# Kernel tuning notes

Hardware: AMD Instinct MI355X
Metric: run time of the kernel (lower is better)

## Reference

```python
import jax, jax.numpy as jnp
import numpy as np

N, S, C, K, V = 8, 2048, 4, 512, 64


def setup_inputs() -> dict:
    key = jax.random.key(0)
    kx, ke = jax.random.split(key)
    x = jax.random.normal(kx, (N, S, C, V), dtype=jnp.float32)
    # nn.Parameter(torch.rand(...)) -> uniform [0,1)
    embedding = jax.random.uniform(ke, (C, K, V), dtype=jnp.float32)
    return {"x": x, "embedding": embedding}


def reference(x, embedding):
    n, s, c, v = x.shape
    xf = x.reshape(n * s, c, v)  # (NS, C, V)
    x2 = jnp.sum(xf * xf, axis=-1, keepdims=True)           # (NS, C, 1)
    e2 = jnp.sum(embedding * embedding, axis=-1)            # (C, K)
    xe = jnp.einsum('ncv,ckv->nck', xf, embedding)          # (NS, C, K)
    d2 = x2 - 2.0 * xe + e2[None]                           # (NS, C, K)
    index = jnp.argmin(d2, axis=2)                          # (NS, C)
    # gather: output[n, c] = embedding[c, index[n, c]]
    output = embedding[jnp.arange(c)[None, :], index]       # (NS, C, V)
    output = output.reshape(x.shape)
    out0 = jax.lax.stop_gradient(output - x) + x            # straight-through
    d1 = jax.lax.stop_gradient(x) - output
    out1 = jnp.sum(d1 * d1, axis=3)                         # (N, S, C)
    d2_ = x - jax.lax.stop_gradient(output)
    out2 = jnp.sum(d2_ * d2_, axis=3)                       # (N, S, C)
    return (out0, out1, out2)
```

## Files before the change

kernel.cpp:

```cpp
#include <hip/hip_runtime.h>

#define NROW 16384
#define CCH  4
#define KCB  512
#define VDIM 64
#define KO   4096

typedef __attribute__((ext_vector_type(8))) short  short8;
typedef __attribute__((ext_vector_type(4))) float  floatx4;

__device__ inline unsigned short bf16h(float v, float* rem) {
    unsigned u = __float_as_uint(v);
    unsigned r = u + 0x7FFFu + ((u >> 16) & 1u);
    unsigned short h = (unsigned short)(r >> 16);
    *rem = v - __uint_as_float((unsigned)h << 16);
    return h;
}

__global__ __launch_bounds__(512, 1)
void vq_fused(const float* __restrict__ x, const float* __restrict__ emb,
              float* __restrict__ out) {
    extern __shared__ unsigned short smem[];
    unsigned short* bhi = smem;
    unsigned short* blo = smem + 32768;
    float* e2s = (float*)(smem + 65536);

    const int tid  = threadIdx.x;
    const int lane = tid & 63;
    const int m    = lane & 15;
    const int quad = lane >> 4;
    const int wave = tid >> 6;
    const int c    = blockIdx.y;
    const int rbase = blockIdx.x * 256 + wave * 32;

    const float* embc = emb + (size_t)c * (KCB * VDIM);

    {
        const int cb = wave * 64;
#pragma unroll
        for (int j = 0; j < 16; ++j) {
            const int g = cb * 16 + j * 64 + lane;
            const float4 t = ((const float4*)embc)[g];
            const int code = cb + j * 4 + quad;
            const int koct = m >> 1, half = m & 1;
            ushort4 h4, l4; float r, d;
            h4.x = bf16h(t.x, &r); l4.x = bf16h(r, &d);
            h4.y = bf16h(t.y, &r); l4.y = bf16h(r, &d);
            h4.z = bf16h(t.z, &r); l4.z = bf16h(r, &d);
            h4.w = bf16h(t.w, &r); l4.w = bf16h(r, &d);
            const int off = (koct * 512 + code) * 8 + half * 4;
            *(ushort4*)&bhi[off] = h4;
            *(ushort4*)&blo[off] = l4;
            float s = 0.f;
            s = fmaf(t.x, t.x, s); s = fmaf(t.y, t.y, s);
            s = fmaf(t.z, t.z, s); s = fmaf(t.w, t.w, s);
            s += __shfl_xor(s, 1, 64);
            s += __shfl_xor(s, 2, 64);
            s += __shfl_xor(s, 4, 64);
            s += __shfl_xor(s, 8, 64);
            if (m == 0) e2s[code] = s;
        }
    }

    short8 ah[2][2], al[2][2];
#pragma unroll
    for (int g = 0; g < 2; ++g) {
        const int row = rbase + g * 16 + m;
        const float4* xr = (const float4*)(x + ((size_t)row * CCH + c) * VDIM);
#pragma unroll
        for (int h = 0; h < 2; ++h) {
            const float4 f0 = xr[h * 8 + quad * 2];
            const float4 f1 = xr[h * 8 + quad * 2 + 1];
            const float fv[8] = {f0.x, f0.y, f0.z, f0.w, f1.x, f1.y, f1.z, f1.w};
            short8 hh, ll;
#pragma unroll
            for (int j = 0; j < 8; ++j) {
                float r, d;
                hh[j] = (short)bf16h(fv[j], &r);
                ll[j] = (short)bf16h(r, &d);
            }
            ah[g][h] = hh; al[g][h] = ll;
        }
    }

    __syncthreads();

    float bd[2][4]; int bkk[2][4];
#pragma unroll
    for (int g = 0; g < 2; ++g)
#pragma unroll
        for (int j = 0; j < 4; ++j) { bd[g][j] = 3.4e38f; bkk[g][j] = 0; }

#pragma unroll 4
    for (int t = 0; t < KCB / 16; ++t) {
        const int code = t * 16 + m;
        const unsigned short* ph = bhi + (size_t)(quad * 512 + code) * 8;
        const unsigned short* pl = blo + (size_t)(quad * 512 + code) * 8;
        const short8 bh0 = *(const short8*)ph;
        const short8 bh1 = *(const short8*)(ph + 4 * KO);
        const short8 bl0 = *(const short8*)pl;
        const short8 bl1 = *(const short8*)(pl + 4 * KO);
        const float e2v = e2s[code];

        floatx4 acch0 = {0.f,0.f,0.f,0.f}, acch1 = {0.f,0.f,0.f,0.f};
        floatx4 accm0 = {0.f,0.f,0.f,0.f}, accm1 = {0.f,0.f,0.f,0.f};
        acch0 = __builtin_amdgcn_mfma_f32_16x16x32_bf16(ah[0][0], bh0, acch0, 0, 0, 0);
        acch1 = __builtin_amdgcn_mfma_f32_16x16x32_bf16(ah[1][0], bh0, acch1, 0, 0, 0);
        accm0 = __builtin_amdgcn_mfma_f32_16x16x32_bf16(ah[0][0], bl0, accm0, 0, 0, 0);
        accm1 = __builtin_amdgcn_mfma_f32_16x16x32_bf16(ah[1][0], bl0, accm1, 0, 0, 0);
        acch0 = __builtin_amdgcn_mfma_f32_16x16x32_bf16(ah[0][1], bh1, acch0, 0, 0, 0);
        acch1 = __builtin_amdgcn_mfma_f32_16x16x32_bf16(ah[1][1], bh1, acch1, 0, 0, 0);
        accm0 = __builtin_amdgcn_mfma_f32_16x16x32_bf16(al[0][0], bh0, accm0, 0, 0, 0);
        accm1 = __builtin_amdgcn_mfma_f32_16x16x32_bf16(al[1][0], bh0, accm1, 0, 0, 0);
        accm0 = __builtin_amdgcn_mfma_f32_16x16x32_bf16(ah[0][1], bl1, accm0, 0, 0, 0);
        accm1 = __builtin_amdgcn_mfma_f32_16x16x32_bf16(ah[1][1], bl1, accm1, 0, 0, 0);
        accm0 = __builtin_amdgcn_mfma_f32_16x16x32_bf16(al[0][1], bh1, accm0, 0, 0, 0);
        accm1 = __builtin_amdgcn_mfma_f32_16x16x32_bf16(al[1][1], bh1, accm1, 0, 0, 0);

#pragma unroll
        for (int j = 0; j < 4; ++j) {
            const float d0 = fmaf(-2.0f, acch0[j] + accm0[j], e2v);
            const float d1 = fmaf(-2.0f, acch1[j] + accm1[j], e2v);
            if (d0 < bd[0][j]) { bd[0][j] = d0; bkk[0][j] = code; }
            if (d1 < bd[1][j]) { bd[1][j] = d1; bkk[1][j] = code; }
        }
    }

#pragma unroll
    for (int g = 0; g < 2; ++g)
#pragma unroll
    for (int j = 0; j < 4; ++j) {
        float d = bd[g][j]; int k = bkk[g][j];
#pragma unroll
        for (int mask = 1; mask < 16; mask <<= 1) {
            const float od = __shfl_xor(d, mask, 64);
            const int   ok = __shfl_xor(k, mask, 64);
            if (od < d || (od == d && ok < k)) { d = od; k = ok; }
        }
        bd[g][j] = d; bkk[g][j] = k;
    }

    const size_t base1 = (size_t)NROW * CCH * VDIM;
    const size_t base2 = base1 + (size_t)NROW * CCH;
#pragma unroll
    for (int g = 0; g < 2; ++g)
#pragma unroll
    for (int j = 0; j < 4; ++j) {
        const int row  = rbase + g * 16 + quad * 4 + j;
        const int code = bkk[g][j];
        const float4 t4 = ((const float4*)(x + ((size_t)row * CCH + c) * VDIM))[m];
        const float4 e4 = ((const float4*)(embc + (size_t)code * VDIM))[m];
        float4 w;
        w.x = (e4.x - t4.x) + t4.x;
        w.y = (e4.y - t4.y) + t4.y;
        w.z = (e4.z - t4.z) + t4.z;
        w.w = (e4.w - t4.w) + t4.w;
        ((float4*)(out + ((size_t)row * CCH + c) * VDIM))[m] = w;
        float s = 0.f, dx;
        dx = t4.x - e4.x; s = fmaf(dx, dx, s);
        dx = t4.y - e4.y; s = fmaf(dx, dx, s);
        dx = t4.z - e4.z; s = fmaf(dx, dx, s);
        dx = t4.w - e4.w; s = fmaf(dx, dx, s);
        s += __shfl_xor(s, 1, 64);
        s += __shfl_xor(s, 2, 64);
        s += __shfl_xor(s, 4, 64);
        s += __shfl_xor(s, 8, 64);
        if (m == 0) {
            const size_t idx = (size_t)row * CCH + c;
            out[base1 + idx] = s;
            out[base2 + idx] = s;
        }
    }
}

extern "C" void kernel_launch(void* const* d_in, const int* in_sizes, int n_in,
                              void* d_out, int out_size, void* d_ws, size_t ws_size,
                              hipStream_t stream) {
    const float* x   = (const float*)d_in[0];
    const float* emb = (const float*)d_in[1];
    float* out = (float*)d_out;
    const size_t lds_bytes = 65536u * 2u + 512u * 4u;
    vq_fused<<<dim3(NROW / 256, CCH), dim3(512), lds_bytes, stream>>>(x, emb, out);
}
```

Baseline: 92.62 us.

## Drop codebook low-part bf16 split, halve rows per block, XOR-swizzle LDS

```diff
diff --git a/kernel.cpp b/kernel.cpp
--- a/kernel.cpp
+++ b/kernel.cpp
@@ -4,7 +4,6 @@
 #define CCH  4
 #define KCB  512
 #define VDIM 64
-#define KO   4096
 
 typedef __attribute__((ext_vector_type(8))) short  short8;
 typedef __attribute__((ext_vector_type(4))) float  floatx4;
@@ -16,14 +15,17 @@
     *rem = v - __uint_as_float((unsigned)h << 16);
     return h;
 }
+__device__ inline unsigned short bf16r(float v) {
+    unsigned u = __float_as_uint(v);
+    return (unsigned short)((u + 0x7FFFu + ((u >> 16) & 1u)) >> 16);
+}
 
-__global__ __launch_bounds__(512, 1)
+__global__ __launch_bounds__(512, 4)
 void vq_fused(const float* __restrict__ x, const float* __restrict__ emb,
               float* __restrict__ out) {
     extern __shared__ unsigned short smem[];
-    unsigned short* bhi = smem;
-    unsigned short* blo = smem + 32768;
-    float* e2s = (float*)(smem + 65536);
+    unsigned short* eh = smem;
+    float* e2s = (float*)(smem + 32768);
 
     const int tid  = threadIdx.x;
     const int lane = tid & 63;
@@ -31,26 +33,23 @@
     const int quad = lane >> 4;
     const int wave = tid >> 6;
     const int c    = blockIdx.y;
-    const int rbase = blockIdx.x * 256 + wave * 32;
+    const int rbase = blockIdx.x * 128 + wave * 16;
 
     const float* embc = emb + (size_t)c * (KCB * VDIM);
 
     {
         const int cb = wave * 64;
+        const int koct = m >> 1, half = m & 1;
 #pragma unroll
         for (int j = 0; j < 16; ++j) {
             const int g = cb * 16 + j * 64 + lane;
             const float4 t = ((const float4*)embc)[g];
             const int code = cb + j * 4 + quad;
-            const int koct = m >> 1, half = m & 1;
-            ushort4 h4, l4; float r, d;
-            h4.x = bf16h(t.x, &r); l4.x = bf16h(r, &d);
-            h4.y = bf16h(t.y, &r); l4.y = bf16h(r, &d);
-            h4.z = bf16h(t.z, &r); l4.z = bf16h(r, &d);
-            h4.w = bf16h(t.w, &r); l4.w = bf16h(r, &d);
-            const int off = (koct * 512 + code) * 8 + half * 4;
-            *(ushort4*)&bhi[off] = h4;
-            *(ushort4*)&blo[off] = l4;
+            ushort4 h4;
+            h4.x = bf16r(t.x); h4.y = bf16r(t.y);
+            h4.z = bf16r(t.z); h4.w = bf16r(t.w);
+            const int off = (koct * 512 + (code ^ koct)) * 8 + half * 4;
+            *(ushort4*)&eh[off] = h4;
             float s = 0.f;
             s = fmaf(t.x, t.x, s); s = fmaf(t.y, t.y, s);
             s = fmaf(t.z, t.z, s); s = fmaf(t.w, t.w, s);
@@ -62,10 +61,9 @@
         }
     }
 
-    short8 ah[2][2], al[2][2];
-#pragma unroll
-    for (int g = 0; g < 2; ++g) {
-        const int row = rbase + g * 16 + m;
+    short8 ah[2], al[2];
+    {
+        const int row = rbase + m;
         const float4* xr = (const float4*)(x + ((size_t)row * CCH + c) * VDIM);
 #pragma unroll
         for (int h = 0; h < 2; ++h) {
@@ -79,75 +77,57 @@
                 hh[j] = (short)bf16h(fv[j], &r);
                 ll[j] = (short)bf16h(r, &d);
             }
-            ah[g][h] = hh; al[g][h] = ll;
+            ah[h] = hh; al[h] = ll;
         }
     }
 
     __syncthreads();
 
-    float bd[2][4]; int bkk[2][4];
+    float bd[4]; int bkk[4];
 #pragma unroll
-    for (int g = 0; g < 2; ++g)
-#pragma unroll
-        for (int j = 0; j < 4; ++j) { bd[g][j] = 3.4e38f; bkk[g][j] = 0; }
+    for (int j = 0; j < 4; ++j) { bd[j] = 3.4e38f; bkk[j] = 0; }
+
+    const int mq0 = m ^ quad;
+    const int mq1 = m ^ (quad + 4);
 
 #pragma unroll 4
     for (int t = 0; t < KCB / 16; ++t) {
         const int code = t * 16 + m;
-        const unsigned short* ph = bhi + (size_t)(quad * 512 + code) * 8;
-        const unsigned short* pl = blo + (size_t)(quad * 512 + code) * 8;
-        const short8 bh0 = *(const short8*)ph;
-        const short8 bh1 = *(const short8*)(ph + 4 * KO);
-        const short8 bl0 = *(const short8*)pl;
-        const short8 bl1 = *(const short8*)(pl + 4 * KO);
+        const short8 bh0 = *(const short8*)&eh[( quad      * 512 + t * 16 + mq0) * 8];
+        const short8 bh1 = *(const short8*)&eh[((quad + 4) * 512 + t * 16 + mq1) * 8];
         const float e2v = e2s[code];
 
-        floatx4 acch0 = {0.f,0.f,0.f,0.f}, acch1 = {0.f,0.f,0.f,0.f};
-        floatx4 accm0 = {0.f,0.f,0.f,0.f}, accm1 = {0.f,0.f,0.f,0.f};
-        acch0 = __builtin_amdgcn_mfma_f32_16x16x32_bf16(ah[0][0], bh0, acch0, 0, 0, 0);
-        acch1 = __builtin_amdgcn_mfma_f32_16x16x32_bf16(ah[1][0], bh0, acch1, 0, 0, 0);
-        accm0 = __builtin_amdgcn_mfma_f32_16x16x32_bf16(ah[0][0], bl0, accm0, 0, 0, 0);
-        accm1 = __builtin_amdgcn_mfma_f32_16x16x32_bf16(ah[1][0], bl0, accm1, 0, 0, 0);
-        acch0 = __builtin_amdgcn_mfma_f32_16x16x32_bf16(ah[0][1], bh1, acch0, 0, 0, 0);
-        acch1 = __builtin_amdgcn_mfma_f32_16x16x32_bf16(ah[1][1], bh1, acch1, 0, 0, 0);
-        accm0 = __builtin_amdgcn_mfma_f32_16x16x32_bf16(al[0][0], bh0, accm0, 0, 0, 0);
-        accm1 = __builtin_amdgcn_mfma_f32_16x16x32_bf16(al[1][0], bh0, accm1, 0, 0, 0);
-        accm0 = __builtin_amdgcn_mfma_f32_16x16x32_bf16(ah[0][1], bl1, accm0, 0, 0, 0);
-        accm1 = __builtin_amdgcn_mfma_f32_16x16x32_bf16(ah[1][1], bl1, accm1, 0, 0, 0);
-        accm0 = __builtin_amdgcn_mfma_f32_16x16x32_bf16(al[0][1], bh1, accm0, 0, 0, 0);
-        accm1 = __builtin_amdgcn_mfma_f32_16x16x32_bf16(al[1][1], bh1, accm1, 0, 0, 0);
+        floatx4 acc0 = {0.f,0.f,0.f,0.f}, acc1 = {0.f,0.f,0.f,0.f};
+        acc0 = __builtin_amdgcn_mfma_f32_16x16x32_bf16(ah[0], bh0, acc0, 0, 0, 0);
+        acc1 = __builtin_amdgcn_mfma_f32_16x16x32_bf16(al[0], bh0, acc1, 0, 0, 0);
+        acc0 = __builtin_amdgcn_mfma_f32_16x16x32_bf16(ah[1], bh1, acc0, 0, 0, 0);
+        acc1 = __builtin_amdgcn_mfma_f32_16x16x32_bf16(al[1], bh1, acc1, 0, 0, 0);
 
 #pragma unroll
         for (int j = 0; j < 4; ++j) {
-            const float d0 = fmaf(-2.0f, acch0[j] + accm0[j], e2v);
-            const float d1 = fmaf(-2.0f, acch1[j] + accm1[j], e2v);
-            if (d0 < bd[0][j]) { bd[0][j] = d0; bkk[0][j] = code; }
-            if (d1 < bd[1][j]) { bd[1][j] = d1; bkk[1][j] = code; }
+            const float d0 = fmaf(-2.0f, acc0[j] + acc1[j], e2v);
+            if (d0 < bd[j]) { bd[j] = d0; bkk[j] = code; }
         }
     }
 
 #pragma unroll
-    for (int g = 0; g < 2; ++g)
-#pragma unroll
     for (int j = 0; j < 4; ++j) {
-        float d = bd[g][j]; int k = bkk[g][j];
+        float d = bd[j]; int k = bkk[j];
 #pragma unroll
         for (int mask = 1; mask < 16; mask <<= 1) {
             const float od = __shfl_xor(d, mask, 64);
             const int   ok = __shfl_xor(k, mask, 64);
             if (od < d || (od == d && ok < k)) { d = od; k = ok; }
         }
-        bd[g][j] = d; bkk[g][j] = k;
+        bd[j] = d; bkk[j] = k;
     }
 
     const size_t base1 = (size_t)NROW * CCH * VDIM;
     const size_t base2 = base1 + (size_t)NROW * CCH;
 #pragma unroll
-    for (int g = 0; g < 2; ++g)
-#pragma unroll
     for (int j = 0; j < 4; ++j) {
-        const int row  = rbase + g * 16 + quad * 4 + j;
-        const int code = bkk[g][j];
+        const int row  = rbase + quad * 4 + j;
+        const int code = bkk[j];
         const float4 t4 = ((const float4*)(x + ((size_t)row * CCH + c) * VDIM))[m];
         const float4 e4 = ((const float4*)(embc + (size_t)code * VDIM))[m];
         float4 w;
@@ -179,6 +159,6 @@
     const float* x   = (const float*)d_in[0];
     const float* emb = (const float*)d_in[1];
     float* out = (float*)d_out;
-    const size_t lds_bytes = 65536u * 2u + 512u * 4u;
-    vq_fused<<<dim3(NROW / 256, CCH), dim3(512), lds_bytes, stream>>>(x, emb, out);
+    const size_t lds_bytes = 65536u + 2048u;
+    vq_fused<<<dim3(NROW / 128, CCH), dim3(512), lds_bytes, stream>>>(x, emb, out);
 }
```

After: 85.33 us. -7.9%, faster.

## Drop codebook low-bf16 term, split codebook across wave halves, swizzle LDS

Applied to the files above, without the earlier changes.

```diff
diff --git a/kernel.cpp b/kernel.cpp
--- a/kernel.cpp
+++ b/kernel.cpp
@@ -4,7 +4,6 @@
 #define CCH  4
 #define KCB  512
 #define VDIM 64
-#define KO   4096
 
 typedef __attribute__((ext_vector_type(8))) short  short8;
 typedef __attribute__((ext_vector_type(4))) float  floatx4;
@@ -16,56 +15,63 @@
     *rem = v - __uint_as_float((unsigned)h << 16);
     return h;
 }
-
-__global__ __launch_bounds__(512, 1)
+__device__ inline unsigned short bf16r(float v) {
+    unsigned u = __float_as_uint(v);
+    return (unsigned short)((u + 0x7FFFu + ((u >> 16) & 1u)) >> 16);
+}
+
+__global__ __launch_bounds__(1024)
 void vq_fused(const float* __restrict__ x, const float* __restrict__ emb,
               float* __restrict__ out) {
-    extern __shared__ unsigned short smem[];
-    unsigned short* bhi = smem;
-    unsigned short* blo = smem + 32768;
-    float* e2s = (float*)(smem + 65536);
+    extern __shared__ char smem[];
+    unsigned short* eh  = (unsigned short*)smem;
+    float*          e2t = (float*)(smem + 65536);
+    float*          sdm = (float*)(smem + 67584);
+    int*            skm = (int*)  (smem + 69632);
 
     const int tid  = threadIdx.x;
     const int lane = tid & 63;
     const int m    = lane & 15;
     const int quad = lane >> 4;
     const int wave = tid >> 6;
+    const int z    = wave >> 3;
+    const int wb   = wave & 7;
     const int c    = blockIdx.y;
-    const int rbase = blockIdx.x * 256 + wave * 32;
+    const int rowblk = blockIdx.x * 256 + wb * 32;
 
     const float* embc = emb + (size_t)c * (KCB * VDIM);
 
     {
-        const int cb = wave * 64;
-#pragma unroll
-        for (int j = 0; j < 16; ++j) {
-            const int g = cb * 16 + j * 64 + lane;
-            const float4 t = ((const float4*)embc)[g];
-            const int code = cb + j * 4 + quad;
-            const int koct = m >> 1, half = m & 1;
-            ushort4 h4, l4; float r, d;
-            h4.x = bf16h(t.x, &r); l4.x = bf16h(r, &d);
-            h4.y = bf16h(t.y, &r); l4.y = bf16h(r, &d);
-            h4.z = bf16h(t.z, &r); l4.z = bf16h(r, &d);
-            h4.w = bf16h(t.w, &r); l4.w = bf16h(r, &d);
-            const int off = (koct * 512 + code) * 8 + half * 4;
-            *(ushort4*)&bhi[off] = h4;
-            *(ushort4*)&blo[off] = l4;
-            float s = 0.f;
-            s = fmaf(t.x, t.x, s); s = fmaf(t.y, t.y, s);
-            s = fmaf(t.z, t.z, s); s = fmaf(t.w, t.w, s);
-            s += __shfl_xor(s, 1, 64);
-            s += __shfl_xor(s, 2, 64);
-            s += __shfl_xor(s, 4, 64);
-            s += __shfl_xor(s, 8, 64);
-            if (m == 0) e2s[code] = s;
+        const int code = tid >> 1, vh = tid & 1;
+        const float4* ef = (const float4*)embc + code * 16 + vh * 8;
+        float4 f[8];
+#pragma unroll
+        for (int j = 0; j < 8; ++j) f[j] = ef[j];
+        float s = 0.f;
+#pragma unroll
+        for (int j = 0; j < 8; ++j) {
+            s = fmaf(f[j].x, f[j].x, s); s = fmaf(f[j].y, f[j].y, s);
+            s = fmaf(f[j].z, f[j].z, s); s = fmaf(f[j].w, f[j].w, s);
+        }
+        s += __shfl_xor(s, 1, 64);
+        if (vh == 0) e2t[(code & 15) * 32 + (code >> 4)] = s;
+#pragma unroll
+        for (int p = 0; p < 4; ++p) {
+            const int koct = vh * 4 + p;
+            const float4 a = f[2 * p], b = f[2 * p + 1];
+            short8 hv;
+            hv[0] = (short)bf16r(a.x); hv[1] = (short)bf16r(a.y);
+            hv[2] = (short)bf16r(a.z); hv[3] = (short)bf16r(a.w);
+            hv[4] = (short)bf16r(b.x); hv[5] = (short)bf16r(b.y);
+            hv[6] = (short)bf16r(b.z); hv[7] = (short)bf16r(b.w);
+            *(short8*)&eh[(koct * 512 + (code ^ koct)) * 8] = hv;
         }
     }
 
     short8 ah[2][2], al[2][2];
 #pragma unroll
     for (int g = 0; g < 2; ++g) {
-        const int row = rbase + g * 16 + m;
+        const int row = rowblk + g * 16 + m;
         const float4* xr = (const float4*)(x + ((size_t)row * CCH + c) * VDIM);
 #pragma unroll
         for (int h = 0; h < 2; ++h) {
@@ -85,45 +91,53 @@
 
     __syncthreads();
 
+    float e2r[16];
+    {
+        const float4* ep = (const float4*)&e2t[m * 32 + z * 16];
+#pragma unroll
+        for (int i = 0; i < 4; ++i) {
+            const float4 v = ep[i];
+            e2r[4*i] = v.x; e2r[4*i+1] = v.y; e2r[4*i+2] = v.z; e2r[4*i+3] = v.w;
+        }
+    }
+
     float bd[2][4]; int bkk[2][4];
 #pragma unroll
     for (int g = 0; g < 2; ++g)
 #pragma unroll
         for (int j = 0; j < 4; ++j) { bd[g][j] = 3.4e38f; bkk[g][j] = 0; }
 
-#pragma unroll 4
-    for (int t = 0; t < KCB / 16; ++t) {
-        const int code = t * 16 + m;
-        const unsigned short* ph = bhi + (size_t)(quad * 512 + code) * 8;
-        const unsigned short* pl = blo + (size_t)(quad * 512 + code) * 8;
-        const short8 bh0 = *(const short8*)ph;
-        const short8 bh1 = *(const short8*)(ph + 4 * KO);
-        const short8 bl0 = *(const short8*)pl;
-        const short8 bl1 = *(const short8*)(pl + 4 * KO);
-        const float e2v = e2s[code];
-
-        floatx4 acch0 = {0.f,0.f,0.f,0.f}, acch1 = {0.f,0.f,0.f,0.f};
-        floatx4 accm0 = {0.f,0.f,0.f,0.f}, accm1 = {0.f,0.f,0.f,0.f};
-        acch0 = __builtin_amdgcn_mfma_f32_16x16x32_bf16(ah[0][0], bh0, acch0, 0, 0, 0);
-        acch1 = __builtin_amdgcn_mfma_f32_16x16x32_bf16(ah[1][0], bh0, acch1, 0, 0, 0);
-        accm0 = __builtin_amdgcn_mfma_f32_16x16x32_bf16(ah[0][0], bl0, accm0, 0, 0, 0);
-        accm1 = __builtin_amdgcn_mfma_f32_16x16x32_bf16(ah[1][0], bl0, accm1, 0, 0, 0);
-        acch0 = __builtin_amdgcn_mfma_f32_16x16x32_bf16(ah[0][1], bh1, acch0, 0, 0, 0);
-        acch1 = __builtin_amdgcn_mfma_f32_16x16x32_bf16(ah[1][1], bh1, acch1, 0, 0, 0);
-        accm0 = __builtin_amdgcn_mfma_f32_16x16x32_bf16(al[0][0], bh0, accm0, 0, 0, 0);
-        accm1 = __builtin_amdgcn_mfma_f32_16x16x32_bf16(al[1][0], bh0, accm1, 0, 0, 0);
-        accm0 = __builtin_amdgcn_mfma_f32_16x16x32_bf16(ah[0][1], bl1, accm0, 0, 0, 0);
-        accm1 = __builtin_amdgcn_mfma_f32_16x16x32_bf16(ah[1][1], bl1, accm1, 0, 0, 0);
-        accm0 = __builtin_amdgcn_mfma_f32_16x16x32_bf16(al[0][1], bh1, accm0, 0, 0, 0);
-        accm1 = __builtin_amdgcn_mfma_f32_16x16x32_bf16(al[1][1], bh1, accm1, 0, 0, 0);
-
+    const int mq0 = m ^ quad, mq1 = m ^ (quad + 4);
+    short8 c0 = *(const short8*)&eh[( quad      * 512 + z * 256 + mq0) * 8];
+    short8 c1 = *(const short8*)&eh[((quad + 4) * 512 + z * 256 + mq1) * 8];
+
+#pragma unroll
+    for (int t = 0; t < 16; ++t) {
+        short8 n0 = c0, n1 = c1;
+        if (t < 15) {
+            const int nb = z * 256 + (t + 1) * 16;
+            n0 = *(const short8*)&eh[( quad      * 512 + nb + mq0) * 8];
+            n1 = *(const short8*)&eh[((quad + 4) * 512 + nb + mq1) * 8];
+        }
+        floatx4 a0 = {0.f,0.f,0.f,0.f}, a1 = {0.f,0.f,0.f,0.f};
+        a0 = __builtin_amdgcn_mfma_f32_16x16x32_bf16(ah[0][0], c0, a0, 0, 0, 0);
+        a1 = __builtin_amdgcn_mfma_f32_16x16x32_bf16(ah[1][0], c0, a1, 0, 0, 0);
+        a0 = __builtin_amdgcn_mfma_f32_16x16x32_bf16(al[0][0], c0, a0, 0, 0, 0);
+        a1 = __builtin_amdgcn_mfma_f32_16x16x32_bf16(al[1][0], c0, a1, 0, 0, 0);
+        a0 = __builtin_amdgcn_mfma_f32_16x16x32_bf16(ah[0][1], c1, a0, 0, 0, 0);
+        a1 = __builtin_amdgcn_mfma_f32_16x16x32_bf16(ah[1][1], c1, a1, 0, 0, 0);
+        a0 = __builtin_amdgcn_mfma_f32_16x16x32_bf16(al[0][1], c1, a0, 0, 0, 0);
+        a1 = __builtin_amdgcn_mfma_f32_16x16x32_bf16(al[1][1], c1, a1, 0, 0, 0);
+
+        const int code = z * 256 + t * 16 + m;
 #pragma unroll
         for (int j = 0; j < 4; ++j) {
-            const float d0 = fmaf(-2.0f, acch0[j] + accm0[j], e2v);
-            const float d1 = fmaf(-2.0f, acch1[j] + accm1[j], e2v);
+            const float d0 = fmaf(-2.0f, a0[j], e2r[t]);
+            const float d1 = fmaf(-2.0f, a1[j], e2r[t]);
             if (d0 < bd[0][j]) { bd[0][j] = d0; bkk[0][j] = code; }
             if (d1 < bd[1][j]) { bd[1][j] = d1; bkk[1][j] = code; }
         }
+        c0 = n0; c1 = n1;
     }
 
 #pragma unroll
@@ -140,14 +154,30 @@
         bd[g][j] = d; bkk[g][j] = k;
     }
 
+    if (m == 0) {
+#pragma unroll
+        for (int g = 0; g < 2; ++g)
+#pragma unroll
+        for (int j = 0; j < 4; ++j) {
+            const int rl = g * 16 + quad * 4 + j;
+            sdm[(z * 8 + wb) * 32 + rl] = bd[g][j];
+            skm[(z * 8 + wb) * 32 + rl] = bkk[g][j];
+        }
+    }
+    __syncthreads();
+
     const size_t base1 = (size_t)NROW * CCH * VDIM;
     const size_t base2 = base1 + (size_t)NROW * CCH;
 #pragma unroll
-    for (int g = 0; g < 2; ++g)
-#pragma unroll
     for (int j = 0; j < 4; ++j) {
-        const int row  = rbase + g * 16 + quad * 4 + j;
-        const int code = bkk[g][j];
+        const int rl  = z * 16 + quad * 4 + j;
+        const float d0 = sdm[(0 * 8 + wb) * 32 + rl];
+        const float d1 = sdm[(1 * 8 + wb) * 32 + rl];
+        const int   k0 = skm[(0 * 8 + wb) * 32 + rl];
+        const int   k1 = skm[(1 * 8 + wb) * 32 + rl];
+        const int code = (d1 < d0) ? k1 : k0;
+        const int row  = rowblk + rl;
+
         const float4 t4 = ((const float4*)(x + ((size_t)row * CCH + c) * VDIM))[m];
         const float4 e4 = ((const float4*)(embc + (size_t)code * VDIM))[m];
         float4 w;
@@ -179,6 +209,6 @@
     const float* x   = (const float*)d_in[0];
     const float* emb = (const float*)d_in[1];
     float* out = (float*)d_out;
-    const size_t lds_bytes = 65536u * 2u + 512u * 4u;
-    vq_fused<<<dim3(NROW / 256, CCH), dim3(512), lds_bytes, stream>>>(x, emb, out);
-}
+    const size_t lds_bytes = 65536u + 2048u + 2048u + 2048u;
+    vq_fused<<<dim3(NROW / 256, CCH), dim3(1024), lds_bytes, stream>>>(x, emb, out);
+}
```

Result: slower. 121.6 us (+31.3%).
